# Kernel tuning notes

Hardware: AMD Instinct MI355X
Metric: run time of the kernel (lower is better)

## Reference

```python
import jax, jax.numpy as jnp
import numpy as np

NF = 64      # num_feat
NFR = 5      # num_frames
G = 8        # offset/deformable groups
CENTER = NFR // 2
K = 9        # 3x3 taps


def conv3x3(x, w, b):
    y = jax.lax.conv_general_dilated(x, w, (1, 1), 'SAME',
                                     dimension_numbers=('NCHW', 'OIHW', 'NCHW'))
    return y + b[None, :, None, None]


def mdcn(x, offsets, masks, w, b):
    # x: [B,C,H,W]; offsets: [B,2*G*K,H,W] (layout g,k,(y,x)); masks: [B,G*K,H,W]
    B, C, H, W = x.shape
    Cg = C // G
    off = offsets.reshape(B, G, K, 2, H, W)
    oy, ox = off[:, :, :, 0], off[:, :, :, 1]          # [B,G,K,H,W]
    m = masks.reshape(B, G, K, H, W)
    ky = jnp.repeat(jnp.arange(3), 3) - 1              # [K]
    kx = jnp.tile(jnp.arange(3), 3) - 1
    base_y = (ky[:, None, None] + jnp.arange(H)[None, :, None]).astype(x.dtype)  # [K,H,1]
    base_x = (kx[:, None, None] + jnp.arange(W)[None, None, :]).astype(x.dtype)  # [K,1,W]
    py = oy + base_y[None, None]                        # [B,G,K,H,W]
    px = ox + base_x[None, None]
    y0f = jnp.floor(py); x0f = jnp.floor(px)
    ty = py - y0f; tx = px - x0f
    y0 = y0f.astype(jnp.int32); x0 = x0f.astype(jnp.int32)
    xg = x.reshape(B, G, Cg, H * W)

    def gather(yi, xi):
        valid = (yi >= 0) & (yi < H) & (xi >= 0) & (xi < W)
        yc = jnp.clip(yi, 0, H - 1); xc = jnp.clip(xi, 0, W - 1)
        idx = (yc * W + xc).reshape(B, G, 1, K * H * W)
        idx = jnp.broadcast_to(idx, (B, G, Cg, K * H * W))
        v = jnp.take_along_axis(xg, idx, axis=3).reshape(B, G, Cg, K, H, W)
        return v * valid.reshape(B, G, 1, K, H, W)

    v00 = gather(y0, x0); v01 = gather(y0, x0 + 1)
    v10 = gather(y0 + 1, x0); v11 = gather(y0 + 1, x0 + 1)
    ty_ = ty[:, :, None]; tx_ = tx[:, :, None]          # [B,G,1,K,H,W]
    samp = (v00 * (1 - ty_) * (1 - tx_) + v01 * (1 - ty_) * tx_ +
            v10 * ty_ * (1 - tx_) + v11 * ty_ * tx_)
    samp = samp * m[:, :, None]                          # modulation
    wr = w.reshape(-1, G, Cg, K)                         # [Cout,G,Cg,K]
    out = jnp.einsum('bgckhw,ogck->bohw', samp, wr)
    return out + b[None, :, None, None]


def setup_inputs():
    key = jax.random.key(0)
    ks = jax.random.split(key, 16)
    def mk(k, shape, fan_in):
        return jax.random.normal(k, shape, jnp.float32) * (1.0 / np.sqrt(fan_in))
    B, H, W = 1, 160, 160
    return {
        'x':   jax.random.normal(ks[0], (B, NFR, 4, H, W), jnp.float32),
        'fw1': mk(ks[1], (NF, 4, 3, 3), 4 * 9),   'fb1': jnp.zeros((NF,), jnp.float32),
        'fw2': mk(ks[2], (NF, NF, 3, 3), NF * 9), 'fb2': jnp.zeros((NF,), jnp.float32),
        'fw3': mk(ks[3], (NF, NF, 3, 3), NF * 9), 'fb3': jnp.zeros((NF,), jnp.float32),
        'ow1': mk(ks[4], (NF, 2 * NF, 3, 3), 2 * NF * 9), 'ob1': jnp.zeros((NF,), jnp.float32),
        'ow2': mk(ks[5], (NF, NF, 3, 3), NF * 9),         'ob2': jnp.zeros((NF,), jnp.float32),
        'ow3': mk(ks[6], (G * 27, NF, 3, 3), NF * 9) * 0.1,
        'ob3': jnp.zeros((G * 27,), jnp.float32),
        'dw':  mk(ks[7], (NF, NF, 3, 3), NF * 9), 'db': jnp.zeros((NF,), jnp.float32),
    }


def reference(x, fw1, fb1, fw2, fb2, fw3, fb3, ow1, ob1, ow2, ob2, ow3, ob3, dw, db):
    B, N, C, H, W = x.shape
    f = x.reshape(B * N, C, H, W)
    f = jax.nn.relu(conv3x3(f, fw1, fb1))
    f = jax.nn.relu(conv3x3(f, fw2, fb2))
    f = jax.nn.relu(conv3x3(f, fw3, fb3))
    feats = f.reshape(B, N, NF, H, W)
    ref = feats[:, CENTER]                               # [B,NF,H,W]
    nc = np.array([i for i in range(N) if i != CENTER])
    curr = feats[:, nc].reshape(B * (N - 1), NF, H, W)
    ref_t = jnp.broadcast_to(ref[:, None], (B, N - 1, NF, H, W)).reshape(B * (N - 1), NF, H, W)
    cat = jnp.concatenate([ref_t, curr], axis=1)         # [B(N-1),2*NF,H,W]
    o = jax.nn.relu(conv3x3(cat, ow1, ob1))
    o = jax.nn.relu(conv3x3(o, ow2, ob2))
    raw = conv3x3(o, ow3, ob3)                           # [B(N-1),27G,H,W]
    offsets = raw[:, :G * 18]
    masks = jax.nn.sigmoid(raw[:, G * 18:])
    aligned = mdcn(curr, offsets, masks, dw, db)
    aligned = aligned.reshape(B, N - 1, NF, H, W)
    return jnp.concatenate([aligned[:, :CENTER], ref[:, None], aligned[:, CENTER:]], axis=1)
```

## Files before the change

kernel.cpp:

```cpp
#include <hip/hip_runtime.h>
#include <hip/hip_bf16.h>
#include <math.h>

#define HH 160
#define WW 160
#define HWsz (HH*WW)

typedef short bf16x8 __attribute__((ext_vector_type(8)));
typedef float f32x4  __attribute__((ext_vector_type(4)));

__device__ inline ushort f2bf(float f) {
    unsigned int u = __float_as_uint(f);
    unsigned int r = (u + 0x7FFFu + ((u >> 16) & 1u)) >> 16;
    return (ushort)r;
}

__device__ inline void unpk8(uint4 u, float* f) {
    f[0] = __uint_as_float(u.x << 16); f[1] = __uint_as_float(u.x & 0xFFFF0000u);
    f[2] = __uint_as_float(u.y << 16); f[3] = __uint_as_float(u.y & 0xFFFF0000u);
    f[4] = __uint_as_float(u.z << 16); f[5] = __uint_as_float(u.z & 0xFFFF0000u);
    f[6] = __uint_as_float(u.w << 16); f[7] = __uint_as_float(u.w & 0xFFFF0000u);
}

__global__ __launch_bounds__(256)
void pack_all(const float* __restrict__ fw2, const float* __restrict__ fw3,
              const float* __restrict__ ow1, const float* __restrict__ ow2,
              const float* __restrict__ ow3, const float* __restrict__ dw,
              ushort* __restrict__ w2p, ushort* __restrict__ w3p,
              ushort* __restrict__ o1p, ushort* __restrict__ o2p,
              ushort* __restrict__ o3p, ushort* __restrict__ wmp)
{
    const int seg = blockIdx.y;
    const int idx = blockIdx.x * 256 + threadIdx.x;

    if (seg == 5) {
        if (idx >= 18 * 4 * 64) return;
        const int lane = idx & 63;
        const int mt   = (idx >> 6) & 3;
        const int chunk = idx >> 8;
        const int o  = mt * 16 + (lane & 15);
        const int gk = chunk * 4 + (lane >> 4);
        const int g  = gk / 9, k = gk % 9;
        ushort v[8];
#pragma unroll
        for (int j = 0; j < 8; ++j)
            v[j] = f2bf(dw[((size_t)o * 64 + g * 8 + j) * 9 + k]);
        uint4 pk;
        pk.x = (unsigned)v[0] | ((unsigned)v[1] << 16);
        pk.y = (unsigned)v[2] | ((unsigned)v[3] << 16);
        pk.z = (unsigned)v[4] | ((unsigned)v[5] << 16);
        pk.w = (unsigned)v[6] | ((unsigned)v[7] << 16);
        *(uint4*)(wmp + (size_t)idx * 8) = pk;
        return;
    }

    const float* w; ushort* wp; int Cout, Cin, MT_TOT, CIC;
    switch (seg) {
        case 0: w = fw2; wp = w2p; Cout = 64;  Cin = 64;  MT_TOT = 4;  CIC = 2; break;
        case 1: w = fw3; wp = w3p; Cout = 64;  Cin = 64;  MT_TOT = 4;  CIC = 2; break;
        case 2: w = ow1; wp = o1p; Cout = 64;  Cin = 128; MT_TOT = 4;  CIC = 4; break;
        case 3: w = ow2; wp = o2p; Cout = 64;  Cin = 64;  MT_TOT = 4;  CIC = 2; break;
        default: w = ow3; wp = o3p; Cout = 216; Cin = 64; MT_TOT = 16; CIC = 2; break;
    }
    const int total = 9 * CIC * MT_TOT * 64;
    if (idx >= total) return;
    const int lane = idx & 63;
    int t = idx >> 6;
    const int mt  = t % MT_TOT; t /= MT_TOT;
    const int cic = t % CIC;    t /= CIC;
    const int tap = t;
    const int co  = mt * 16 + (lane & 15);
    const int ci0 = cic * 32 + (lane >> 4) * 8;
    ushort v[8];
#pragma unroll
    for (int j = 0; j < 8; ++j) {
        const int ci = ci0 + j;
        float f = 0.f;
        if (co < Cout && ci < Cin) f = w[((size_t)co * Cin + ci) * 9 + tap];
        v[j] = f2bf(f);
    }
    uint4 pk;
    pk.x = (unsigned)v[0] | ((unsigned)v[1] << 16);
    pk.y = (unsigned)v[2] | ((unsigned)v[3] << 16);
    pk.z = (unsigned)v[4] | ((unsigned)v[5] << 16);
    pk.w = (unsigned)v[6] | ((unsigned)v[7] << 16);
    *(uint4*)(wp + (size_t)idx * 8) = pk;
}

template<int CI_STEPS, bool CONCAT, bool RELU, int OMODE>
__global__ __launch_bounds__(256, 3)
void mfma_conv(const ushort* __restrict__ in, const ushort* __restrict__ wp,
               const float* __restrict__ bias, void* __restrict__ outv,
               int Cout, int MT_TOT, int COG,
               float* __restrict__ outmain, ushort* __restrict__ aux)
{
    constexpr int ROWS = 8, HR = ROWS + 2, NT = 4;
    constexpr int C8   = 8;
    constexpr int CICT = 2 * CI_STEPS;
    constexpr int CIN  = CICT * 32;
    __shared__ uint4 s_in4[HR * 34 * C8];
    __shared__ uint4 s_a4[2][256];

    const int tid = threadIdx.x;
    const int lane = tid & 63, wid = tid >> 6;
    const int lane15 = lane & 15, lgrp = lane >> 4;
    const int bz = blockIdx.z;
    const int frame = bz / COG, cog = bz % COG;
    const int x0 = blockIdx.x * 32, y0 = blockIdx.y * ROWS;

    const ushort* src = nullptr; const ushort* srcRef = nullptr; const ushort* srcCur = nullptr;
    if (CONCAT) {
        const int fidx = (frame < 2) ? frame : frame + 1;
        srcRef = in + (size_t)2 * HWsz * 64;
        srcCur = in + (size_t)fidx * HWsz * 64;
    } else {
        src = in + (size_t)frame * HWsz * CIN;
    }

    f32x4 acc[4][NT];
#pragma unroll
    for (int m = 0; m < 4; ++m)
#pragma unroll
        for (int n = 0; n < NT; ++n) acc[m][n] = (f32x4){0.f, 0.f, 0.f, 0.f};

    const uint4* wp4 = (const uint4*)wp;
    const int wrow = wid * 2;
    const int mtg0 = cog * 4;
    const int amt = tid >> 6, aln = tid & 63;

#pragma unroll
    for (int step = 0; step < CI_STEPS; ++step) {
        uint4 areg = wp4[((size_t)(0 * CICT + step * 2 + 0) * MT_TOT + mtg0 + amt) * 64 + aln];
        for (int i = tid; i < HR * 34 * C8; i += 256) {
            const int ci8l = i & (C8 - 1);
            const int rem = i / C8;
            const int col = rem % 34, row = rem / 34;
            const int gy = y0 + row - 1, gx = x0 + col - 1;
            const int gci8 = step * C8 + ci8l;
            uint4 v = {0u, 0u, 0u, 0u};
            if (gy >= 0 && gy < HH && gx >= 0 && gx < WW) {
                if (CONCAT) {
                    const ushort* sp = (gci8 < 8) ? srcRef : srcCur;
                    v = *(const uint4*)(sp + (size_t)(gy * WW + gx) * 64 + (gci8 & 7) * 8);
                } else {
                    v = *(const uint4*)(src + (size_t)(gy * WW + gx) * CIN + gci8 * 8);
                }
            }
            s_in4[(row * 34 + col) * C8 + (ci8l ^ (col & 7))] = v;
        }
        s_a4[0][tid] = areg;
        __syncthreads();

#pragma unroll
        for (int kk = 0; kk < 18; ++kk) {
            const int tap = kk >> 1, cic = kk & 1;
            const int dy  = tap / 3 - 1;
            const int dxp = tap % 3;
            uint4 nreg;
            if (kk < 17) {
                const int ntap = (kk + 1) >> 1, ncic = (kk + 1) & 1;
                nreg = wp4[((size_t)(ntap * CICT + step * 2 + ncic) * MT_TOT + mtg0 + amt) * 64 + aln];
            }
            bf16x8 a[4];
#pragma unroll
            for (int mt = 0; mt < 4; ++mt)
                a[mt] = *(const bf16x8*)&s_a4[kk & 1][mt * 64 + lane];
#pragma unroll
            for (int nt = 0; nt < NT; ++nt) {
                const int row_l = wrow + (nt >> 1) + dy + 1;
                const int col_l = (nt & 1) * 16 + lane15 + dxp;
                const bf16x8 b = *(const bf16x8*)
                    &s_in4[(row_l * 34 + col_l) * C8 + ((cic * 4 + lgrp) ^ (col_l & 7))];
#pragma unroll
                for (int mt = 0; mt < 4; ++mt)
                    acc[mt][nt] = __builtin_amdgcn_mfma_f32_16x16x32_bf16(a[mt], b, acc[mt][nt], 0, 0, 0);
            }
            if (kk < 17) s_a4[(kk + 1) & 1][tid] = nreg;
            __syncthreads();
        }
    }

#pragma unroll
    for (int mt = 0; mt < 4; ++mt) {
        const int co = cog * 64 + mt * 16 + lgrp * 4;
        if (co < Cout) {
            const float4 bs = *(const float4*)&bias[co];
#pragma unroll
            for (int nt = 0; nt < NT; ++nt) {
                const int yy = y0 + wrow + (nt >> 1);
                const int xx = x0 + (nt & 1) * 16 + lane15;
                const int hw = yy * WW + xx;
                f32x4 v = acc[mt][nt];
                v[0] += bs.x; v[1] += bs.y; v[2] += bs.z; v[3] += bs.w;
                if (RELU) {
                    v[0] = fmaxf(v[0], 0.f); v[1] = fmaxf(v[1], 0.f);
                    v[2] = fmaxf(v[2], 0.f); v[3] = fmaxf(v[3], 0.f);
                }
                if (OMODE <= 1) {
                    uint2 pk;
                    pk.x = (unsigned)f2bf(v[0]) | ((unsigned)f2bf(v[1]) << 16);
                    pk.y = (unsigned)f2bf(v[2]) | ((unsigned)f2bf(v[3]) << 16);
                    *(uint2*)((ushort*)outv + ((size_t)frame * HWsz + hw) * 64 + co) = pk;
                    if (OMODE == 1) {
                        if (frame == 2) {
#pragma unroll
                            for (int j = 0; j < 4; ++j)
                                outmain[((size_t)(128 + co + j)) * HWsz + hw] = v[j];
                        } else {
                            const int b = (frame < 2) ? frame : frame - 1;
                            *(uint2*)(aux + (((size_t)(b * 8 + (co >> 3)) * HWsz + hw) * 8 + (co & 7))) = pk;
                        }
                    }
                } else {
                    if (co < 144) {
                        const ushort h0 = f2bf(v[0]), h1 = f2bf(v[1]);
                        const ushort h2 = f2bf(v[2]), h3 = f2bf(v[3]);
                        unsigned* roff = (unsigned*)outv + (size_t)frame * 72 * HWsz;
                        roff[(size_t)(co >> 1) * HWsz + hw]       = (unsigned)h0 | ((unsigned)h1 << 16);
                        roff[(size_t)((co >> 1) + 1) * HWsz + hw] = (unsigned)h2 | ((unsigned)h3 << 16);
                    } else {
                        ushort* rmsk = aux + (size_t)frame * 72 * HWsz;
                        const int gk0 = co - 144;
#pragma unroll
                        for (int j = 0; j < 4; ++j) {
                            const float m = 1.f / (1.f + __expf(-v[j]));
                            rmsk[(size_t)(gk0 + j) * HWsz + hw] = f2bf(m);
                        }
                    }
                }
            }
        }
    }
}

__global__ __launch_bounds__(256)
void conv1_kernel(const float* __restrict__ x, const float* __restrict__ w,
                  const float* __restrict__ b, ushort* __restrict__ out)
{
    const int fr = blockIdx.z;
    const int t = threadIdx.x;
    const int tx = t & 15, ty = t >> 4;
    const int x0 = blockIdx.x * 16, y0 = blockIdx.y * 16;

    __shared__ float s_x[4][18][18];
    __shared__ float s_w[36][64];
    __shared__ float s_b[64];

    for (int i = t; i < 4 * 18 * 18; i += 256) {
        const int ci = i / 324, rem = i % 324;
        const int yy = rem / 18, xx = rem % 18;
        const int gy = y0 + yy - 1, gx = x0 + xx - 1;
        float v = 0.f;
        if (gy >= 0 && gy < HH && gx >= 0 && gx < WW)
            v = x[((size_t)fr * 4 + ci) * HWsz + gy * WW + gx];
        s_x[ci][yy][xx] = v;
    }
    for (int i = t; i < 36 * 64; i += 256) {
        const int row = i / 64, o = i % 64;
        const int ci = row / 9, tap = row % 9;
        s_w[row][o] = w[((size_t)o * 4 + ci) * 9 + tap];
    }
    if (t < 64) s_b[t] = b[t];
    __syncthreads();

    float acc[64];
#pragma unroll
    for (int i = 0; i < 64; ++i) acc[i] = 0.f;

#pragma unroll
    for (int ci = 0; ci < 4; ++ci) {
#pragma unroll
        for (int tap = 0; tap < 9; ++tap) {
            const float v = s_x[ci][ty + tap / 3][tx + tap % 3];
            const float4* wr = (const float4*)&s_w[ci * 9 + tap][0];
#pragma unroll
            for (int o4 = 0; o4 < 16; ++o4) {
                const float4 wv = wr[o4];
                acc[o4 * 4 + 0] = fmaf(v, wv.x, acc[o4 * 4 + 0]);
                acc[o4 * 4 + 1] = fmaf(v, wv.y, acc[o4 * 4 + 1]);
                acc[o4 * 4 + 2] = fmaf(v, wv.z, acc[o4 * 4 + 2]);
                acc[o4 * 4 + 3] = fmaf(v, wv.w, acc[o4 * 4 + 3]);
            }
        }
    }

    ushort* ob = out + ((size_t)fr * HWsz + (y0 + ty) * WW + (x0 + tx)) * 64;
#pragma unroll
    for (int o8 = 0; o8 < 8; ++o8) {
        ushort v[8];
#pragma unroll
        for (int j = 0; j < 8; ++j)
            v[j] = f2bf(fmaxf(acc[o8 * 8 + j] + s_b[o8 * 8 + j], 0.f));
        uint4 pk;
        pk.x = (unsigned)v[0] | ((unsigned)v[1] << 16);
        pk.y = (unsigned)v[2] | ((unsigned)v[3] << 16);
        pk.z = (unsigned)v[4] | ((unsigned)v[5] << 16);
        pk.w = (unsigned)v[6] | ((unsigned)v[7] << 16);
        *(uint4*)(ob + o8 * 8) = pk;
    }
}

__global__ __launch_bounds__(512, 4)
void mdcn_mfma(const ushort* __restrict__ ftsg, const unsigned* __restrict__ roffg,
               const ushort* __restrict__ rmskg,
               const ushort* __restrict__ wmp, const float* __restrict__ db,
               float* __restrict__ out)
{
    __shared__ uint4 s_w4[18 * 4 * 64];

    const int b    = blockIdx.z;
    const int fidx = (b < 2) ? b : b + 1;
    const int tid  = threadIdx.x;
    const int lane = tid & 63, wid = tid >> 6;
    const int lane15 = lane & 15, lgrp = lane >> 4;
    const int x = blockIdx.x * 16 + lane15;
    const int y = blockIdx.y * 8 + wid;
    const int hw = y * WW + x;

    const uint4* wmp4 = (const uint4*)wmp;
    for (int i = tid; i < 18 * 4 * 64; i += 512) s_w4[i] = wmp4[i];

    const unsigned* roff = roffg + (size_t)b * 72 * HWsz;
    const ushort*   rmsk = rmskg + (size_t)b * 72 * HWsz;

    unsigned opv[18];
#pragma unroll
    for (int n = 0; n < 18; ++n)
        opv[n] = roff[(size_t)(n * 4 + lgrp) * HWsz + hw];

    __syncthreads();

    f32x4 acc[4];
#pragma unroll
    for (int m = 0; m < 4; ++m) acc[m] = (f32x4){0.f, 0.f, 0.f, 0.f};

    auto prep = [&](int n, uint4& u00, uint4& u01, uint4& u10, uint4& u11,
                    float& w00, float& w01, float& w10, float& w11) {
        const int gk = n * 4 + lgrp;
        const int gg = gk / 9, k9 = gk - 9 * gg;
        const int kyy = k9 / 3 - 1, kxx = k9 - (k9 / 3) * 3 - 1;
        const unsigned op = opv[n];
        const float oy = __uint_as_float(op << 16);
        const float ox = __uint_as_float(op & 0xFFFF0000u);
        const float mv = __uint_as_float((unsigned)rmsk[(size_t)gk * HWsz + hw] << 16);

        const float py = oy + (float)(y + kyy);
        const float px = ox + (float)(x + kxx);
        const float y0f = floorf(py), x0f = floorf(px);
        const float tyf = py - y0f, txf = px - x0f;
        const int y0 = (int)y0f, x0i = (int)x0f;
        const int y1 = y0 + 1, x1 = x0i + 1;
        const bool vy0 = (y0 >= 0) & (y0 < HH);
        const bool vy1 = (y1 >= 0) & (y1 < HH);
        const bool vx0 = (x0i >= 0) & (x0i < WW);
        const bool vx1 = (x1 >= 0) & (x1 < WW);
        const int yc0 = min(max(y0, 0), HH - 1), yc1 = min(max(y1, 0), HH - 1);
        const int xc0 = min(max(x0i, 0), WW - 1), xc1 = min(max(x1, 0), WW - 1);
        const float a0 = (1.f - tyf) * mv, a1 = tyf * mv;
        w00 = a0 * (1.f - txf);
        w01 = a0 * txf;
        w10 = a1 * (1.f - txf);
        w11 = a1 * txf;
        if (!(vy0 && vx0)) w00 = 0.f;
        if (!(vy0 && vx1)) w01 = 0.f;
        if (!(vy1 && vx0)) w10 = 0.f;
        if (!(vy1 && vx1)) w11 = 0.f;

        const ushort* pb = ftsg + (size_t)(b * 8 + gg) * HWsz * 8;
        u00 = *(const uint4*)(pb + (size_t)(yc0 * WW + xc0) * 8);
        u01 = *(const uint4*)(pb + (size_t)(yc0 * WW + xc1) * 8);
        u10 = *(const uint4*)(pb + (size_t)(yc1 * WW + xc0) * 8);
        u11 = *(const uint4*)(pb + (size_t)(yc1 * WW + xc1) * 8);
    };

    uint4 cu00, cu01, cu10, cu11;
    float cw00, cw01, cw10, cw11;
    prep(0, cu00, cu01, cu10, cu11, cw00, cw01, cw10, cw11);

#pragma unroll
    for (int g = 0; g < 18; ++g) {
        uint4 nu00, nu01, nu10, nu11;
        float nw00, nw01, nw10, nw11;
        if (g < 17)
            prep(g + 1, nu00, nu01, nu10, nu11, nw00, nw01, nw10, nw11);

        float f00[8], f01[8], f10[8], f11[8];
        unpk8(cu00, f00); unpk8(cu01, f01); unpk8(cu10, f10); unpk8(cu11, f11);
        float s[8];
#pragma unroll
        for (int c = 0; c < 8; ++c)
            s[c] = fmaf(cw11, f11[c], fmaf(cw10, f10[c],
                    fmaf(cw01, f01[c], cw00 * f00[c])));
        uint4 bpk;
        asm("v_cvt_pk_bf16_f32 %0, %1, %2" : "=v"(bpk.x) : "v"(s[0]), "v"(s[1]));
        asm("v_cvt_pk_bf16_f32 %0, %1, %2" : "=v"(bpk.y) : "v"(s[2]), "v"(s[3]));
        asm("v_cvt_pk_bf16_f32 %0, %1, %2" : "=v"(bpk.z) : "v"(s[4]), "v"(s[5]));
        asm("v_cvt_pk_bf16_f32 %0, %1, %2" : "=v"(bpk.w) : "v"(s[6]), "v"(s[7]));
        const bf16x8 bfrag = __builtin_bit_cast(bf16x8, bpk);

#pragma unroll
        for (int mt = 0; mt < 4; ++mt) {
            const bf16x8 a = *(const bf16x8*)&s_w4[(g * 4 + mt) * 64 + lane];
            acc[mt] = __builtin_amdgcn_mfma_f32_16x16x32_bf16(a, bfrag, acc[mt], 0, 0, 0);
        }

        if (g < 17) {
            cu00 = nu00; cu01 = nu01; cu10 = nu10; cu11 = nu11;
            cw00 = nw00; cw01 = nw01; cw10 = nw10; cw11 = nw11;
        }
    }

    float* ob = out + (size_t)fidx * 64 * HWsz + hw;
#pragma unroll
    for (int mt = 0; mt < 4; ++mt) {
        const int o0 = mt * 16 + lgrp * 4;
        const float4 bs = *(const float4*)&db[o0];
        ob[(size_t)(o0 + 0) * HWsz] = acc[mt][0] + bs.x;
        ob[(size_t)(o0 + 1) * HWsz] = acc[mt][1] + bs.y;
        ob[(size_t)(o0 + 2) * HWsz] = acc[mt][2] + bs.z;
        ob[(size_t)(o0 + 3) * HWsz] = acc[mt][3] + bs.w;
    }
}

extern "C" void kernel_launch(void* const* d_in, const int* in_sizes, int n_in,
                              void* d_out, int out_size, void* d_ws, size_t ws_size,
                              hipStream_t stream)
{
    const float* x   = (const float*)d_in[0];
    const float* fw1 = (const float*)d_in[1];
    const float* fb1 = (const float*)d_in[2];
    const float* fw2 = (const float*)d_in[3];
    const float* fb2 = (const float*)d_in[4];
    const float* fw3 = (const float*)d_in[5];
    const float* fb3 = (const float*)d_in[6];
    const float* ow1 = (const float*)d_in[7];
    const float* ob1 = (const float*)d_in[8];
    const float* ow2 = (const float*)d_in[9];
    const float* ob2 = (const float*)d_in[10];
    const float* ow3 = (const float*)d_in[11];
    const float* ob3 = (const float*)d_in[12];
    const float* dw  = (const float*)d_in[13];
    const float* db  = (const float*)d_in[14];
    float* out = (float*)d_out;

    ushort* buf1 = (ushort*)d_ws;
    ushort* buf2 = buf1 + (size_t)5 * HWsz * 64;
    ushort* fts  = buf2 + (size_t)5 * HWsz * 64;
    ushort* ftsg = fts + (size_t)5 * HWsz * 64;
    unsigned* roff = (unsigned*)(ftsg + (size_t)4 * 8 * HWsz * 8);
    ushort* rmsk = (ushort*)(roff + (size_t)4 * 72 * HWsz);
    ushort* w2p  = rmsk + (size_t)4 * 72 * HWsz;
    ushort* w3p  = w2p + 36864;
    ushort* o1p  = w3p + 36864;
    ushort* o2p  = o1p + 73728;
    ushort* o3p  = o2p + 36864;
    ushort* wmp  = o3p + 147456;

    const dim3 blk(256);

    pack_all<<<dim3(72, 6), blk, 0, stream>>>(fw2, fw3, ow1, ow2, ow3, dw,
                                              w2p, w3p, o1p, o2p, o3p, wmp);

    conv1_kernel<<<dim3(10, 10, 5), blk, 0, stream>>>(x, fw1, fb1, buf1);
    mfma_conv<1, false, true, 0><<<dim3(5, 20, 5), blk, 0, stream>>>(
        buf1, w2p, fb2, buf2, 64, 4, 1, nullptr, nullptr);
    mfma_conv<1, false, true, 1><<<dim3(5, 20, 5), blk, 0, stream>>>(
        buf2, w3p, fb3, fts, 64, 4, 1, out, ftsg);

    mfma_conv<2, true, true, 0><<<dim3(5, 20, 4), blk, 0, stream>>>(
        fts, o1p, ob1, buf1, 64, 4, 1, nullptr, nullptr);
    mfma_conv<1, false, true, 0><<<dim3(5, 20, 4), blk, 0, stream>>>(
        buf1, o2p, ob2, buf2, 64, 4, 1, nullptr, nullptr);
    mfma_conv<1, false, false, 3><<<dim3(5, 20, 16), blk, 0, stream>>>(
        buf2, o3p, ob3, roff, 216, 16, 4, nullptr, rmsk);

    mdcn_mfma<<<dim3(10, 20, 4), dim3(512), 0, stream>>>(ftsg, roff, rmsk, wmp, db, out);
}
```

Before: 222.9 us.

## Stage nine weight slices per barrier to cut per-tap syncs in MFMA conv

The conv kernel now loads nine weight fragments at once into a larger double-buffered LDS area and prefetches the next half-step's nine into registers. This cuts the barrier count from one per tap to one per nine taps (plus one after input staging). The cost is about 72KB of weight LDS and 9 extra uint4 registers per thread, so launch bounds drop to 1 block per SM and occupancy falls.

```diff
diff --git a/kernel.cpp b/kernel.cpp
--- a/kernel.cpp
+++ b/kernel.cpp
@@ -88,7 +88,7 @@
 }
 
 template<int CI_STEPS, bool CONCAT, bool RELU, int OMODE>
-__global__ __launch_bounds__(256, 3)
+__global__ __launch_bounds__(256, 1)
 void mfma_conv(const ushort* __restrict__ in, const ushort* __restrict__ wp,
                const float* __restrict__ bias, void* __restrict__ outv,
                int Cout, int MT_TOT, int COG,
@@ -98,8 +98,9 @@
     constexpr int C8   = 8;
     constexpr int CICT = 2 * CI_STEPS;
     constexpr int CIN  = CICT * 32;
+    constexpr int NH   = CI_STEPS * 2;
     __shared__ uint4 s_in4[HR * 34 * C8];
-    __shared__ uint4 s_a4[2][256];
+    __shared__ uint4 s_a4[2][9 * 256];
 
     const int tid = threadIdx.x;
     const int lane = tid & 63, wid = tid >> 6;
@@ -126,11 +127,15 @@
     const uint4* wp4 = (const uint4*)wp;
     const int wrow = wid * 2;
     const int mtg0 = cog * 4;
-    const int amt = tid >> 6, aln = tid & 63;
-
-#pragma unroll
-    for (int step = 0; step < CI_STEPS; ++step) {
-        uint4 areg = wp4[((size_t)(0 * CICT + step * 2 + 0) * MT_TOT + mtg0 + amt) * 64 + aln];
+    const int amt = (tid >> 6) & 3, aln = tid & 63;
+
+    auto aidx = [&](int hh, int it) -> size_t {
+        const int kkg = (hh & 1) * 9 + it;
+        const int tap = kkg >> 1, cic = kkg & 1;
+        return ((size_t)(tap * CICT + (hh >> 1) * 2 + cic) * MT_TOT + mtg0 + amt) * 64 + aln;
+    };
+
+    auto stage_input = [&](int step) {
         for (int i = tid; i < HR * 34 * C8; i += 256) {
             const int ci8l = i & (C8 - 1);
             const int rem = i / C8;
@@ -148,23 +153,41 @@
             }
             s_in4[(row * 34 + col) * C8 + (ci8l ^ (col & 7))] = v;
         }
-        s_a4[0][tid] = areg;
-        __syncthreads();
-
-#pragma unroll
-        for (int kk = 0; kk < 18; ++kk) {
-            const int tap = kk >> 1, cic = kk & 1;
+    };
+
+    uint4 pref[9];
+#pragma unroll
+    for (int it = 0; it < 9; ++it) pref[it] = wp4[aidx(0, it)];
+    stage_input(0);
+#pragma unroll
+    for (int it = 0; it < 9; ++it) s_a4[0][tid + it * 256] = pref[it];
+    if (NH > 1) {
+#pragma unroll
+        for (int it = 0; it < 9; ++it) pref[it] = wp4[aidx(1, it)];
+    }
+    __syncthreads();
+
+#pragma unroll
+    for (int hh = 0; hh < NH; ++hh) {
+        if (hh + 1 < NH) {
+#pragma unroll
+            for (int it = 0; it < 9; ++it)
+                s_a4[(hh + 1) & 1][tid + it * 256] = pref[it];
+            if (hh + 2 < NH) {
+#pragma unroll
+                for (int it = 0; it < 9; ++it) pref[it] = wp4[aidx(hh + 2, it)];
+            }
+        }
+#pragma unroll
+        for (int kkl = 0; kkl < 9; ++kkl) {
+            const int kkg = (hh & 1) * 9 + kkl;
+            const int tap = kkg >> 1, cic = kkg & 1;
             const int dy  = tap / 3 - 1;
             const int dxp = tap % 3;
-            uint4 nreg;
-            if (kk < 17) {
-                const int ntap = (kk + 1) >> 1, ncic = (kk + 1) & 1;
-                nreg = wp4[((size_t)(ntap * CICT + step * 2 + ncic) * MT_TOT + mtg0 + amt) * 64 + aln];
-            }
             bf16x8 a[4];
 #pragma unroll
             for (int mt = 0; mt < 4; ++mt)
-                a[mt] = *(const bf16x8*)&s_a4[kk & 1][mt * 64 + lane];
+                a[mt] = *(const bf16x8*)&s_a4[hh & 1][kkl * 256 + mt * 64 + lane];
 #pragma unroll
             for (int nt = 0; nt < NT; ++nt) {
                 const int row_l = wrow + (nt >> 1) + dy + 1;
@@ -175,7 +198,10 @@
                 for (int mt = 0; mt < 4; ++mt)
                     acc[mt][nt] = __builtin_amdgcn_mfma_f32_16x16x32_bf16(a[mt], b, acc[mt][nt], 0, 0, 0);
             }
-            if (kk < 17) s_a4[(kk + 1) & 1][tid] = nreg;
+        }
+        __syncthreads();
+        if (((hh & 1) == 1) && (hh + 1 < NH)) {
+            stage_input((hh + 1) >> 1);
             __syncthreads();
         }
     }
```

Result: slower. 319.2 us (+43.2%).
